# Optimization experiments

Hardware: AMD Instinct MI355X
Metric: run time of the kernel (lower is better)

The kernel has to match this reference:

```python
import jax, jax.numpy as jnp
import numpy as np
from jax.scipy.linalg import solve_triangular

SPARSITY = 5
COMMITMENT_COST = 0.25
EMBEDDING_DIM = 64
NUM_EMBEDDINGS = 512


def setup_inputs() -> dict:
    key = jax.random.key(0)
    k1, k2 = jax.random.split(key)
    z_e = jax.random.normal(k1, (64, EMBEDDING_DIM, 32, 32), dtype=jnp.float32)
    D = jax.random.normal(k2, (EMBEDDING_DIM, NUM_EMBEDDINGS), dtype=jnp.float32)
    # torch module normalizes atoms in-place (no grad through normalization)
    D = D / jnp.linalg.norm(D, axis=0)
    return {"z_e": z_e, "dictionary": D}


def _batch_omp(signals, D, sparsity):
    # signals: [C, N], D: [C, K]
    C, N = signals.shape
    dtype = signals.dtype
    G = D.T @ D                       # [K, K] Gram matrix
    init_corr = (D.T @ signals).T     # [N, K]
    corr = init_corr
    coeffs = jnp.zeros_like(init_corr)
    L = jnp.ones((N, 1, 1), dtype=dtype)
    omega = jnp.ones(init_corr.shape, dtype=bool)
    I = jnp.zeros((N, 0), dtype=jnp.int32)
    rows = jnp.arange(N)
    for k in range(1, sparsity + 1):
        # argmax atom selection (omega masks already-selected atoms)
        k_hats = jnp.argmax(jnp.abs(corr) * omega, axis=1)        # [N]
        omega = omega.at[rows, k_hats].set(False)
        if k > 1:
            # progressive Cholesky update: G_[n, j] = G[I[n, j], k_hats[n]]
            G_ = G[I, k_hats[:, None]][..., None]                  # [N, k-1, 1]
            w = solve_triangular(L, G_, lower=True)                # [N, k-1, 1]
            w_row = w.reshape(N, 1, k - 1)                         # [N, 1, k-1]
            w_br = jnp.sqrt(1.0 - jnp.sum(w_row ** 2, axis=2, keepdims=True))
            k_zeros = jnp.zeros((N, k - 1, 1), dtype=dtype)
            top = jnp.concatenate([L, k_zeros], axis=2)            # [N, k-1, k]
            bot = jnp.concatenate([w_row, w_br], axis=2)           # [N, 1, k]
            L = jnp.concatenate([top, bot], axis=1)                # [N, k, k]
        I = jnp.concatenate([I, k_hats[:, None].astype(jnp.int32)], axis=1)  # [N, k]
        b = jnp.take_along_axis(init_corr, I, axis=1)[..., None]   # [N, k, 1]
        # cholesky_solve(b, L): solve L L^T x = b
        y = solve_triangular(L, b, lower=True)
        x = solve_triangular(jnp.swapaxes(L, -1, -2), y, lower=False)  # [N, k, 1]
        xs = x[..., 0]                                             # [N, k]
        coeffs = coeffs.at[rows[:, None], I].set(xs)
        beta = jnp.einsum('nk,nkm->nm', xs, G[I])                  # [N, K]
        corr = init_corr - beta
    return coeffs.T                                                # [K, N]


def reference(z_e, dictionary):
    # z_e: [B, C, H, W] -> BHWC, then raw view as [C, B*H*W] (faithful to torch .view)
    z = jnp.transpose(z_e, (0, 2, 3, 1))
    input_shape = z.shape
    zf = z.reshape(EMBEDDING_DIM, -1)
    coeffs = _batch_omp(zf, dictionary, SPARSITY)                  # [K, N]
    z_dl = (dictionary @ coeffs).reshape(input_shape)
    e_latent_loss = jnp.mean((jax.lax.stop_gradient(z_dl) - z) ** 2)
    dl_latent_loss = jnp.mean((z_dl - jax.lax.stop_gradient(z)) ** 2)
    loss = COMMITMENT_COST * e_latent_loss + dl_latent_loss
    z_st = z + jax.lax.stop_gradient(z_dl - z)                     # straight-through
    return jnp.transpose(z_st, (0, 3, 1, 2)), loss, coeffs
```

## Files before the change

kernel.cpp:

```cpp
#include <hip/hip_runtime.h>

#define NSIG  65536
#define KAT   512
#define CDIM  64

typedef float f32x4 __attribute__((ext_vector_type(4)));

__device__ __forceinline__ f32x4 splat4(float x) { return (f32x4){x, x, x, x}; }
__device__ __forceinline__ float bcastf(float v, int l) {
  return __int_as_float(__builtin_amdgcn_readlane(__float_as_int(v), l));
}
__device__ __forceinline__ unsigned umaxu(unsigned a, unsigned b) {
  return a > b ? a : b;
}
__device__ __forceinline__ unsigned dppmax(unsigned v, const int ctrl) {
  switch (ctrl) {
    case 0xB1:  return umaxu(v, (unsigned)__builtin_amdgcn_mov_dpp((int)v, 0xB1, 0xF, 0xF, true));
    case 0x4E:  return umaxu(v, (unsigned)__builtin_amdgcn_mov_dpp((int)v, 0x4E, 0xF, 0xF, true));
    case 0x124: return umaxu(v, (unsigned)__builtin_amdgcn_mov_dpp((int)v, 0x124, 0xF, 0xF, true));
    case 0x128: return umaxu(v, (unsigned)__builtin_amdgcn_mov_dpp((int)v, 0x128, 0xF, 0xF, true));
    case 0x142: return umaxu(v, (unsigned)__builtin_amdgcn_mov_dpp((int)v, 0x142, 0xF, 0xF, true));
    default:    return umaxu(v, (unsigned)__builtin_amdgcn_mov_dpp((int)v, 0x143, 0xF, 0xF, true));
  }
}

__global__ void k_gram(const float* __restrict__ D, float* __restrict__ G,
                       float* __restrict__ DT) {
  int tid = blockIdx.x * 256 + threadIdx.x;
  int i = tid >> 9, j = tid & 511;
  float acc = 0.f;
  #pragma unroll 8
  for (int c = 0; c < CDIM; ++c) acc = fmaf(D[c * KAT + i], D[c * KAT + j], acc);
  G[tid] = acc;
  if (tid < KAT * CDIM) {
    int k = tid >> 6, c = tid & 63;
    DT[tid] = D[c * KAT + k];
  }
}

__global__ void k_tr(const float* __restrict__ ze, float* __restrict__ st) {
  __shared__ float tile[64][33];
  int cz = blockIdx.x >> 5;
  int h  = blockIdx.x & 31;
  int t  = threadIdx.x;
  #pragma unroll
  for (int q = 0; q < 8; ++q) {
    int idx = q * 256 + t;
    int b = idx >> 5, w = idx & 31;
    tile[b][w] = ze[b * 65536 + cz * 1024 + h * 32 + w];
  }
  __syncthreads();
  #pragma unroll
  for (int q = 0; q < 8; ++q) {
    int idx = q * 256 + t;
    int w = idx >> 6, b = idx & 63;
    st[(h * 2048 + w * 64 + cz) * 64 + b] = tile[b][w];
  }
}

#define DECLV(p) f32x4 p##03 = {0,0,0,0}, p##47 = {0,0,0,0}
#define FMA8V(p, sc)                                                   \
  { f32x4 s4 = splat4(sc);                                             \
    p##03 = __builtin_elementwise_fma(d03, s4, p##03);                 \
    p##47 = __builtin_elementwise_fma(d47, s4, p##47); }
#define SEL8V(e, v03, v47)                                             \
  e = v03[0];                                                          \
  e = (jj == 1) ? v03[1] : e; e = (jj == 2) ? v03[2] : e;              \
  e = (jj == 3) ? v03[3] : e; e = (jj == 4) ? v47[0] : e;              \
  e = (jj == 5) ? v47[1] : e; e = (jj == 6) ? v47[2] : e;              \
  e = (jj == 7) ? v47[3] : e

__device__ __forceinline__ float omp_one(
    f32x4& c03, f32x4& c47,
    float* __restrict__ QW,
    const float* __restrict__ G, const float* __restrict__ DT,
    float* __restrict__ coeffs,
    int n, int lane, float zv) {
  int omega = 0xFF;
  int I0 = 0, I1 = 0, I2 = 0, I3 = 0, I4 = 0;
  float L10 = 0, L20 = 0, L21 = 0;
  float L30 = 0, L31 = 0, L32 = 0;
  float L40 = 0, L41 = 0, L42 = 0, L43 = 0;
  float d1v = 1.f, d2v = 1.f, d3v = 1.f, d4v = 1.f;
  float y0v = 0, y1v = 0, y2v = 0, y3v = 0, y4v = 0;
  DECLV(Qa); DECLV(Qb); DECLV(Qc); DECLV(Qd);

  f32x4* QW4 = reinterpret_cast<f32x4*>(QW);

  #pragma unroll
  for (int it = 0; it < 5; ++it) {
    unsigned ab0 = (omega & 1)        ? (__float_as_uint(c03[0]) & 0x7FFFFFFFu) : 0u;
    unsigned ab1 = ((omega >> 1) & 1) ? (__float_as_uint(c03[1]) & 0x7FFFFFFFu) : 0u;
    unsigned ab2 = ((omega >> 2) & 1) ? (__float_as_uint(c03[2]) & 0x7FFFFFFFu) : 0u;
    unsigned ab3 = ((omega >> 3) & 1) ? (__float_as_uint(c03[3]) & 0x7FFFFFFFu) : 0u;
    unsigned ab4 = ((omega >> 4) & 1) ? (__float_as_uint(c47[0]) & 0x7FFFFFFFu) : 0u;
    unsigned ab5 = ((omega >> 5) & 1) ? (__float_as_uint(c47[1]) & 0x7FFFFFFFu) : 0u;
    unsigned ab6 = ((omega >> 6) & 1) ? (__float_as_uint(c47[2]) & 0x7FFFFFFFu) : 0u;
    unsigned ab7 = ((omega >> 7) & 1) ? (__float_as_uint(c47[3]) & 0x7FFFFFFFu) : 0u;
    unsigned la = umaxu(umaxu(umaxu(ab0, ab1), umaxu(ab2, ab3)),
                        umaxu(umaxu(ab4, ab5), umaxu(ab6, ab7)));
    unsigned rmax = la;
    rmax = dppmax(rmax, 0xB1);
    rmax = dppmax(rmax, 0x4E);
    rmax = dppmax(rmax, 0x124);
    rmax = dppmax(rmax, 0x128);
    rmax = dppmax(rmax, 0x142);
    rmax = dppmax(rmax, 0x143);
    unsigned gmu = (unsigned)__builtin_amdgcn_readlane((int)rmax, 63);
    unsigned long long ball = __ballot(la == gmu);
    const int sl = __ffsll((long long)ball) - 1;
    int jb = 7;
    jb = (ab6 == gmu) ? 6 : jb;
    jb = (ab5 == gmu) ? 5 : jb;
    jb = (ab4 == gmu) ? 4 : jb;
    jb = (ab3 == gmu) ? 3 : jb;
    jb = (ab2 == gmu) ? 2 : jb;
    jb = (ab1 == gmu) ? 1 : jb;
    jb = (ab0 == gmu) ? 0 : jb;
    const int jj = __builtin_amdgcn_readlane(jb, sl) & 7;
    const int khat = (sl << 3) | jj;
    if (lane == sl) omega &= ~(1 << jj);

    const int eoff = ((khat >> 2) & 1) * 256 + (khat >> 3) * 4 + (khat & 3);
    float w0 = 0.f, w1 = 0.f, w2 = 0.f, w3 = 0.f;
    if (it > 0) w0 = QW[eoff];
    if (it > 1) w1 = QW[512 + eoff];
    if (it > 2) w2 = QW[1024 + eoff];
    if (it > 3) { float e; SEL8V(e, Qd03, Qd47); w3 = bcastf(e, sl); }

    f32x4 na = {0, 0, 0, 0}, nbv = {0, 0, 0, 0};
    if (it < 4) {
      na  = *reinterpret_cast<const f32x4*>(G + khat * KAT + 8 * lane);
      nbv = *reinterpret_cast<const f32x4*>(G + khat * KAT + 8 * lane + 4);
    }

    float crv;
    { float e; SEL8V(e, c03, c47); crv = bcastf(e, sl); }

    float s2 = 1.f - w0 * w0 - w1 * w1 - w2 * w2 - w3 * w3;
    float dn = __builtin_amdgcn_rsqf(s2);
    float yn = crv * dn;
    if (it == 0) { I0 = khat; y0v = yn; }
    if (it == 1) { I1 = khat; y1v = yn; L10 = w0; d1v = dn; }
    if (it == 2) { I2 = khat; y2v = yn; L20 = w0; L21 = w1; d2v = dn; }
    if (it == 3) { I3 = khat; y3v = yn; L30 = w0; L31 = w1; L32 = w2; d3v = dn; }
    if (it == 4) { I4 = khat; y4v = yn; L40 = w0; L41 = w1; L42 = w2; L43 = w3; d4v = dn; }

    if (it < 4) {
      f32x4 qn03 = na, qn47 = nbv;
      if (it > 0) {
        f32x4 w4 = splat4(-w0);
        qn03 = __builtin_elementwise_fma(w4, Qa03, qn03);
        qn47 = __builtin_elementwise_fma(w4, Qa47, qn47);
      }
      if (it > 1) {
        f32x4 w4 = splat4(-w1);
        qn03 = __builtin_elementwise_fma(w4, Qb03, qn03);
        qn47 = __builtin_elementwise_fma(w4, Qb47, qn47);
      }
      if (it > 2) {
        f32x4 w4 = splat4(-w2);
        qn03 = __builtin_elementwise_fma(w4, Qc03, qn03);
        qn47 = __builtin_elementwise_fma(w4, Qc47, qn47);
      }
      f32x4 dn4 = splat4(dn);
      qn03 = qn03 * dn4;
      qn47 = qn47 * dn4;
      if (it < 3) {
        QW4[it * 128 + lane]      = qn03;
        QW4[it * 128 + 64 + lane] = qn47;
      }
      if (it == 0) { Qa03 = qn03; Qa47 = qn47; }
      if (it == 1) { Qb03 = qn03; Qb47 = qn47; }
      if (it == 2) { Qc03 = qn03; Qc47 = qn47; }
      if (it == 3) { Qd03 = qn03; Qd47 = qn47; }
      f32x4 yn4 = splat4(-yn);
      c03 = __builtin_elementwise_fma(yn4, qn03, c03);
      c47 = __builtin_elementwise_fma(yn4, qn47, c47);
    }
  }

  float x4 = y4v * d4v;
  float x3 = (y3v - L43 * x4) * d3v;
  float x2 = (y2v - L32 * x3 - L42 * x4) * d2v;
  float x1 = (y1v - L21 * x2 - L31 * x3 - L41 * x4) * d1v;
  float x0 =  y0v - L10 * x1 - L20 * x2 - L30 * x3 - L40 * x4;

  if (lane < 5) {
    int It = I0; float xt = x0;
    if (lane == 1) { It = I1; xt = x1; }
    if (lane == 2) { It = I2; xt = x2; }
    if (lane == 3) { It = I3; xt = x3; }
    if (lane == 4) { It = I4; xt = x4; }
    coeffs[(long)It * NSIG + n] = xt;
  }
  float rec = x0 * DT[I0 * 64 + lane];
  rec = fmaf(x1, DT[I1 * 64 + lane], rec);
  rec = fmaf(x2, DT[I2 * 64 + lane], rec);
  rec = fmaf(x3, DT[I3 * 64 + lane], rec);
  rec = fmaf(x4, DT[I4 * 64 + lane], rec);
  return rec - zv;
}

__global__ __launch_bounds__(64) void k_omp(
    const float* __restrict__ D, const float* __restrict__ G,
    const float* __restrict__ DT, const float* __restrict__ ST,
    float* __restrict__ out0, float* __restrict__ lossp,
    float* __restrict__ coeffs) {
  __shared__ float QL[3][512];
  const int lane = threadIdx.x;
  const int wid  = blockIdx.x;
  const int cc = wid >> 7;
  const int w3 = wid & 127;
  const int nbase = cc + 512 * w3;
  const float* Dp = D + 8 * lane;
  float* QW = &QL[0][0];
  float lossacc = 0.f;

  const int n0 = nbase;             const int n1 = nbase + 64;
  const int n2 = nbase + 128;       const int n3 = nbase + 192;
  const int n4 = nbase + 256;       const int n5 = nbase + 320;
  const int n6 = nbase + 384;       const int n7 = nbase + 448;
  float svA = ST[n0 * 64 + lane];
  float svB = ST[n1 * 64 + lane];
  float svC = ST[n2 * 64 + lane];
  float svD = ST[n3 * 64 + lane];
  float svE = ST[n4 * 64 + lane];
  float svF = ST[n5 * 64 + lane];
  float svG = ST[n6 * 64 + lane];
  float svH = ST[n7 * 64 + lane];

  DECLV(cA); DECLV(cB); DECLV(cC); DECLV(cD);
  DECLV(cE); DECLV(cF); DECLV(cG); DECLV(cH);

  #pragma unroll 2
  for (int r = 0; r < 64; ++r) {
    const f32x4 d03 = *reinterpret_cast<const f32x4*>(Dp + r * KAT);
    const f32x4 d47 = *reinterpret_cast<const f32x4*>(Dp + r * KAT + 4);
    const float sA = bcastf(svA, r);
    const float sB = bcastf(svB, r);
    const float sC = bcastf(svC, r);
    const float sD = bcastf(svD, r);
    const float sE = bcastf(svE, r);
    const float sF = bcastf(svF, r);
    const float sG = bcastf(svG, r);
    const float sH = bcastf(svH, r);
    FMA8V(cA, sA) FMA8V(cB, sB) FMA8V(cC, sC) FMA8V(cD, sD)
    FMA8V(cE, sE) FMA8V(cF, sF) FMA8V(cG, sG) FMA8V(cH, sH)
  }

  float dA = omp_one(cA03, cA47, QW, G, DT, coeffs, n0, lane, svA);
  lossacc = fmaf(dA, dA, lossacc);
  float dB = omp_one(cB03, cB47, QW, G, DT, coeffs, n1, lane, svB);
  lossacc = fmaf(dB, dB, lossacc);
  float dC = omp_one(cC03, cC47, QW, G, DT, coeffs, n2, lane, svC);
  lossacc = fmaf(dC, dC, lossacc);
  float dD = omp_one(cD03, cD47, QW, G, DT, coeffs, n3, lane, svD);
  lossacc = fmaf(dD, dD, lossacc);
  float dE = omp_one(cE03, cE47, QW, G, DT, coeffs, n4, lane, svE);
  lossacc = fmaf(dE, dE, lossacc);
  float dF = omp_one(cF03, cF47, QW, G, DT, coeffs, n5, lane, svF);
  lossacc = fmaf(dF, dF, lossacc);
  float dG = omp_one(cG03, cG47, QW, G, DT, coeffs, n6, lane, svG);
  lossacc = fmaf(dG, dG, lossacc);
  float dH = omp_one(cH03, cH47, QW, G, DT, coeffs, n7, lane, svH);
  lossacc = fmaf(dH, dH, lossacc);

  const int obase = lane * 65536 + cc * 1024 + (w3 >> 2) * 32 + (w3 & 3) * 8;
  *reinterpret_cast<float4*>(out0 + obase) =
      make_float4(svA + dA, svB + dB, svC + dC, svD + dD);
  *reinterpret_cast<float4*>(out0 + obase + 4) =
      make_float4(svE + dE, svF + dF, svG + dG, svH + dH);

  #pragma unroll
  for (int off = 32; off > 0; off >>= 1) lossacc += __shfl_xor(lossacc, off);
  if (lane == 0) atomicAdd(lossp, lossacc * (1.25f / 4194304.f));
}

extern "C" void kernel_launch(void* const* d_in, const int* in_sizes, int n_in,
                              void* d_out, int out_size, void* d_ws, size_t ws_size,
                              hipStream_t stream) {
  const float* ze = (const float*)d_in[0];
  const float* D  = (const float*)d_in[1];
  float* out0 = (float*)d_out;
  float* lossp = out0 + 4194304;
  float* coeffs = out0 + 4194305;

  float* wsf = (float*)d_ws;
  float* G  = wsf;
  float* DT = wsf + 262144;
  float* ST = wsf + 294912;

  (void)hipMemsetAsync((char*)d_out + 16777216ull, 0, 134217732ull, stream);

  hipLaunchKernelGGL(k_gram, dim3(1024), dim3(256), 0, stream, D, G, DT);
  hipLaunchKernelGGL(k_tr,   dim3(2048), dim3(256), 0, stream, ze, ST);
  hipLaunchKernelGGL(k_omp,  dim3(8192), dim3(64), 0, stream,
                     D, G, DT, ST, out0, lossp, coeffs);
}
```

Measured before the change: 173.8 us.

## Process two signals per wavefront, one per 32-lane half, in OMP kernel

Splits each 64-lane wavefront into two halves that each run OMP for a separate signal, with every lane holding 16 correlations instead of 8. The argmax reduction stops at 32 lanes, and Q vectors from earlier iterations now live in shared memory instead of registers. The aim is to halve the serial OMP iteration chains per wave and cut the reduction steps. In exchange each lane does twice the per-element work, shared-memory traffic grows, and register pressure may rise.

```diff
diff --git a/kernel.cpp b/kernel.cpp
--- a/kernel.cpp
+++ b/kernel.cpp
@@ -9,6 +9,9 @@
 __device__ __forceinline__ f32x4 splat4(float x) { return (f32x4){x, x, x, x}; }
 __device__ __forceinline__ float bcastf(float v, int l) {
   return __int_as_float(__builtin_amdgcn_readlane(__float_as_int(v), l));
+}
+__device__ __forceinline__ int bcasti(int v, int l) {
+  return __builtin_amdgcn_readlane(v, l);
 }
 __device__ __forceinline__ unsigned umaxu(unsigned a, unsigned b) {
   return a > b ? a : b;
@@ -19,8 +22,7 @@
     case 0x4E:  return umaxu(v, (unsigned)__builtin_amdgcn_mov_dpp((int)v, 0x4E, 0xF, 0xF, true));
     case 0x124: return umaxu(v, (unsigned)__builtin_amdgcn_mov_dpp((int)v, 0x124, 0xF, 0xF, true));
     case 0x128: return umaxu(v, (unsigned)__builtin_amdgcn_mov_dpp((int)v, 0x128, 0xF, 0xF, true));
-    case 0x142: return umaxu(v, (unsigned)__builtin_amdgcn_mov_dpp((int)v, 0x142, 0xF, 0xF, true));
-    default:    return umaxu(v, (unsigned)__builtin_amdgcn_mov_dpp((int)v, 0x143, 0xF, 0xF, true));
+    default:    return umaxu(v, (unsigned)__builtin_amdgcn_mov_dpp((int)v, 0x142, 0xF, 0xF, true));
   }
 }
 
@@ -58,125 +60,172 @@
   }
 }
 
-#define DECLV(p) f32x4 p##03 = {0,0,0,0}, p##47 = {0,0,0,0}
-#define FMA8V(p, sc)                                                   \
-  { f32x4 s4 = splat4(sc);                                             \
-    p##03 = __builtin_elementwise_fma(d03, s4, p##03);                 \
-    p##47 = __builtin_elementwise_fma(d47, s4, p##47); }
-#define SEL8V(e, v03, v47)                                             \
-  e = v03[0];                                                          \
-  e = (jj == 1) ? v03[1] : e; e = (jj == 2) ? v03[2] : e;              \
-  e = (jj == 3) ? v03[3] : e; e = (jj == 4) ? v47[0] : e;              \
-  e = (jj == 5) ? v47[1] : e; e = (jj == 6) ? v47[2] : e;              \
-  e = (jj == 7) ? v47[3] : e
-
-__device__ __forceinline__ float omp_one(
-    f32x4& c03, f32x4& c47,
+#define SEL16(e, v0, v1, v2, v3, idx)                                   \
+  e = v0[0];                                                            \
+  e = ((idx) == 1) ? v0[1] : e;  e = ((idx) == 2) ? v0[2] : e;          \
+  e = ((idx) == 3) ? v0[3] : e;  e = ((idx) == 4) ? v1[0] : e;          \
+  e = ((idx) == 5) ? v1[1] : e;  e = ((idx) == 6) ? v1[2] : e;          \
+  e = ((idx) == 7) ? v1[3] : e;  e = ((idx) == 8) ? v2[0] : e;          \
+  e = ((idx) == 9) ? v2[1] : e;  e = ((idx) == 10) ? v2[2] : e;         \
+  e = ((idx) == 11) ? v2[3] : e; e = ((idx) == 12) ? v3[0] : e;         \
+  e = ((idx) == 13) ? v3[1] : e; e = ((idx) == 14) ? v3[2] : e;         \
+  e = ((idx) == 15) ? v3[3] : e;
+
+__device__ __forceinline__ void omp_pair(
+    f32x4& c0, f32x4& c1, f32x4& c2, f32x4& c3,
     float* __restrict__ QW,
     const float* __restrict__ G, const float* __restrict__ DT,
     float* __restrict__ coeffs,
-    int n, int lane, float zv) {
-  int omega = 0xFF;
-  int I0 = 0, I1 = 0, I2 = 0, I3 = 0, I4 = 0;
-  float L10 = 0, L20 = 0, L21 = 0;
-  float L30 = 0, L31 = 0, L32 = 0;
-  float L40 = 0, L41 = 0, L42 = 0, L43 = 0;
-  float d1v = 1.f, d2v = 1.f, d3v = 1.f, d4v = 1.f;
-  float y0v = 0, y1v = 0, y2v = 0, y3v = 0, y4v = 0;
-  DECLV(Qa); DECLV(Qb); DECLV(Qc); DECLV(Qd);
+    int nP, int nQ, int lane, float svP, float svQ,
+    float& dP_out, float& dQ_out) {
+  const int hl = lane & 31;
+  const bool loHalf = lane < 32;
+  const int sb4 = loHalf ? 0 : 384;
+  unsigned omega = 0xFFFFu;
+  int IA0=0, IA1=0, IA2=0, IA3=0, IA4=0;
+  int IB0=0, IB1=0, IB2=0, IB3=0, IB4=0;
+  float L10=0, L20=0, L21=0, L30=0, L31=0, L32=0;
+  float L40=0, L41=0, L42=0, L43=0;
+  float d1v=1.f, d2v=1.f, d3v=1.f, d4v=1.f;
+  float y0v=0, y1v=0, y2v=0, y3v=0, y4v=0;
+  f32x4 Qd0={0,0,0,0}, Qd1={0,0,0,0}, Qd2={0,0,0,0}, Qd3={0,0,0,0};
 
   f32x4* QW4 = reinterpret_cast<f32x4*>(QW);
 
   #pragma unroll
   for (int it = 0; it < 5; ++it) {
-    unsigned ab0 = (omega & 1)        ? (__float_as_uint(c03[0]) & 0x7FFFFFFFu) : 0u;
-    unsigned ab1 = ((omega >> 1) & 1) ? (__float_as_uint(c03[1]) & 0x7FFFFFFFu) : 0u;
-    unsigned ab2 = ((omega >> 2) & 1) ? (__float_as_uint(c03[2]) & 0x7FFFFFFFu) : 0u;
-    unsigned ab3 = ((omega >> 3) & 1) ? (__float_as_uint(c03[3]) & 0x7FFFFFFFu) : 0u;
-    unsigned ab4 = ((omega >> 4) & 1) ? (__float_as_uint(c47[0]) & 0x7FFFFFFFu) : 0u;
-    unsigned ab5 = ((omega >> 5) & 1) ? (__float_as_uint(c47[1]) & 0x7FFFFFFFu) : 0u;
-    unsigned ab6 = ((omega >> 6) & 1) ? (__float_as_uint(c47[2]) & 0x7FFFFFFFu) : 0u;
-    unsigned ab7 = ((omega >> 7) & 1) ? (__float_as_uint(c47[3]) & 0x7FFFFFFFu) : 0u;
-    unsigned la = umaxu(umaxu(umaxu(ab0, ab1), umaxu(ab2, ab3)),
-                        umaxu(umaxu(ab4, ab5), umaxu(ab6, ab7)));
+    unsigned ab0  = (omega & 1u)          ? (__float_as_uint(c0[0]) & 0x7FFFFFFFu) : 0u;
+    unsigned ab1  = ((omega >> 1) & 1u)   ? (__float_as_uint(c0[1]) & 0x7FFFFFFFu) : 0u;
+    unsigned ab2  = ((omega >> 2) & 1u)   ? (__float_as_uint(c0[2]) & 0x7FFFFFFFu) : 0u;
+    unsigned ab3  = ((omega >> 3) & 1u)   ? (__float_as_uint(c0[3]) & 0x7FFFFFFFu) : 0u;
+    unsigned ab4  = ((omega >> 4) & 1u)   ? (__float_as_uint(c1[0]) & 0x7FFFFFFFu) : 0u;
+    unsigned ab5  = ((omega >> 5) & 1u)   ? (__float_as_uint(c1[1]) & 0x7FFFFFFFu) : 0u;
+    unsigned ab6  = ((omega >> 6) & 1u)   ? (__float_as_uint(c1[2]) & 0x7FFFFFFFu) : 0u;
+    unsigned ab7  = ((omega >> 7) & 1u)   ? (__float_as_uint(c1[3]) & 0x7FFFFFFFu) : 0u;
+    unsigned ab8  = ((omega >> 8) & 1u)   ? (__float_as_uint(c2[0]) & 0x7FFFFFFFu) : 0u;
+    unsigned ab9  = ((omega >> 9) & 1u)   ? (__float_as_uint(c2[1]) & 0x7FFFFFFFu) : 0u;
+    unsigned ab10 = ((omega >> 10) & 1u)  ? (__float_as_uint(c2[2]) & 0x7FFFFFFFu) : 0u;
+    unsigned ab11 = ((omega >> 11) & 1u)  ? (__float_as_uint(c2[3]) & 0x7FFFFFFFu) : 0u;
+    unsigned ab12 = ((omega >> 12) & 1u)  ? (__float_as_uint(c3[0]) & 0x7FFFFFFFu) : 0u;
+    unsigned ab13 = ((omega >> 13) & 1u)  ? (__float_as_uint(c3[1]) & 0x7FFFFFFFu) : 0u;
+    unsigned ab14 = ((omega >> 14) & 1u)  ? (__float_as_uint(c3[2]) & 0x7FFFFFFFu) : 0u;
+    unsigned ab15 = ((omega >> 15) & 1u)  ? (__float_as_uint(c3[3]) & 0x7FFFFFFFu) : 0u;
+    unsigned la = umaxu(
+        umaxu(umaxu(umaxu(ab0, ab1), umaxu(ab2, ab3)),
+              umaxu(umaxu(ab4, ab5), umaxu(ab6, ab7))),
+        umaxu(umaxu(umaxu(ab8, ab9), umaxu(ab10, ab11)),
+              umaxu(umaxu(ab12, ab13), umaxu(ab14, ab15))));
     unsigned rmax = la;
     rmax = dppmax(rmax, 0xB1);
     rmax = dppmax(rmax, 0x4E);
     rmax = dppmax(rmax, 0x124);
     rmax = dppmax(rmax, 0x128);
     rmax = dppmax(rmax, 0x142);
-    rmax = dppmax(rmax, 0x143);
-    unsigned gmu = (unsigned)__builtin_amdgcn_readlane((int)rmax, 63);
+    unsigned gA = (unsigned)bcasti((int)rmax, 31);
+    unsigned gB = (unsigned)bcasti((int)rmax, 63);
+    unsigned gmu = loHalf ? gA : gB;
     unsigned long long ball = __ballot(la == gmu);
-    const int sl = __ffsll((long long)ball) - 1;
-    int jb = 7;
-    jb = (ab6 == gmu) ? 6 : jb;
-    jb = (ab5 == gmu) ? 5 : jb;
-    jb = (ab4 == gmu) ? 4 : jb;
-    jb = (ab3 == gmu) ? 3 : jb;
-    jb = (ab2 == gmu) ? 2 : jb;
-    jb = (ab1 == gmu) ? 1 : jb;
-    jb = (ab0 == gmu) ? 0 : jb;
-    const int jj = __builtin_amdgcn_readlane(jb, sl) & 7;
-    const int khat = (sl << 3) | jj;
-    if (lane == sl) omega &= ~(1 << jj);
-
-    const int eoff = ((khat >> 2) & 1) * 256 + (khat >> 3) * 4 + (khat & 3);
+    const int slA = __ffsll((long long)(ball & 0xFFFFFFFFull)) - 1;
+    const int slB = 32 + __ffsll((long long)(ball >> 32)) - 1;
+    int jb = 15;
+    jb = (ab14 == gmu) ? 14 : jb;
+    jb = (ab13 == gmu) ? 13 : jb;
+    jb = (ab12 == gmu) ? 12 : jb;
+    jb = (ab11 == gmu) ? 11 : jb;
+    jb = (ab10 == gmu) ? 10 : jb;
+    jb = (ab9  == gmu) ? 9  : jb;
+    jb = (ab8  == gmu) ? 8  : jb;
+    jb = (ab7  == gmu) ? 7  : jb;
+    jb = (ab6  == gmu) ? 6  : jb;
+    jb = (ab5  == gmu) ? 5  : jb;
+    jb = (ab4  == gmu) ? 4  : jb;
+    jb = (ab3  == gmu) ? 3  : jb;
+    jb = (ab2  == gmu) ? 2  : jb;
+    jb = (ab1  == gmu) ? 1  : jb;
+    jb = (ab0  == gmu) ? 0  : jb;
+    const int jjA = bcasti(jb, slA) & 15;
+    const int jjB = bcasti(jb, slB) & 15;
+    const int khatA = ((slA & 31) << 4) | jjA;
+    const int khatB = ((slB & 31) << 4) | jjB;
+    if (lane == slA || lane == slB) omega &= ~(1u << (jb & 15));
+
+    const int eoffA = ((khatA & 15) >> 2) * 128 + (khatA >> 4) * 4 + (khatA & 3);
+    const int eoffB = ((khatB & 15) >> 2) * 128 + (khatB >> 4) * 4 + (khatB & 3);
+    const int hbase = loHalf ? eoffA : (1536 + eoffB);
     float w0 = 0.f, w1 = 0.f, w2 = 0.f, w3 = 0.f;
-    if (it > 0) w0 = QW[eoff];
-    if (it > 1) w1 = QW[512 + eoff];
-    if (it > 2) w2 = QW[1024 + eoff];
-    if (it > 3) { float e; SEL8V(e, Qd03, Qd47); w3 = bcastf(e, sl); }
-
-    f32x4 na = {0, 0, 0, 0}, nbv = {0, 0, 0, 0};
+    if (it > 0) w0 = QW[hbase];
+    if (it > 1) w1 = QW[hbase + 512];
+    if (it > 2) w2 = QW[hbase + 1024];
+    if (it > 3) {
+      float e; SEL16(e, Qd0, Qd1, Qd2, Qd3, jb)
+      float eA = bcastf(e, slA), eB = bcastf(e, slB);
+      w3 = loHalf ? eA : eB;
+    }
+
+    const int khat_l = loHalf ? khatA : khatB;
+    const float* Gp = G + khat_l * KAT + hl * 16;
+    f32x4 na = {0,0,0,0}, nb = {0,0,0,0}, nc = {0,0,0,0}, nd = {0,0,0,0};
     if (it < 4) {
-      na  = *reinterpret_cast<const f32x4*>(G + khat * KAT + 8 * lane);
-      nbv = *reinterpret_cast<const f32x4*>(G + khat * KAT + 8 * lane + 4);
+      na = *reinterpret_cast<const f32x4*>(Gp);
+      nb = *reinterpret_cast<const f32x4*>(Gp + 4);
+      nc = *reinterpret_cast<const f32x4*>(Gp + 8);
+      nd = *reinterpret_cast<const f32x4*>(Gp + 12);
     }
 
     float crv;
-    { float e; SEL8V(e, c03, c47); crv = bcastf(e, sl); }
-
-    float s2 = 1.f - w0 * w0 - w1 * w1 - w2 * w2 - w3 * w3;
-    float dn = __builtin_amdgcn_rsqf(s2);
+    {
+      float e; SEL16(e, c0, c1, c2, c3, jb)
+      float eA = bcastf(e, slA), eB = bcastf(e, slB);
+      crv = loHalf ? eA : eB;
+    }
+
+    float s2v = 1.f - w0 * w0 - w1 * w1 - w2 * w2 - w3 * w3;
+    float dn = __builtin_amdgcn_rsqf(s2v);
     float yn = crv * dn;
-    if (it == 0) { I0 = khat; y0v = yn; }
-    if (it == 1) { I1 = khat; y1v = yn; L10 = w0; d1v = dn; }
-    if (it == 2) { I2 = khat; y2v = yn; L20 = w0; L21 = w1; d2v = dn; }
-    if (it == 3) { I3 = khat; y3v = yn; L30 = w0; L31 = w1; L32 = w2; d3v = dn; }
-    if (it == 4) { I4 = khat; y4v = yn; L40 = w0; L41 = w1; L42 = w2; L43 = w3; d4v = dn; }
+    if (it == 0) { IA0 = khatA; IB0 = khatB; y0v = yn; }
+    if (it == 1) { IA1 = khatA; IB1 = khatB; y1v = yn; L10 = w0; d1v = dn; }
+    if (it == 2) { IA2 = khatA; IB2 = khatB; y2v = yn; L20 = w0; L21 = w1; d2v = dn; }
+    if (it == 3) { IA3 = khatA; IB3 = khatB; y3v = yn; L30 = w0; L31 = w1; L32 = w2; d3v = dn; }
+    if (it == 4) { IA4 = khatA; IB4 = khatB; y4v = yn; L40 = w0; L41 = w1; L42 = w2; L43 = w3; d4v = dn; }
 
     if (it < 4) {
-      f32x4 qn03 = na, qn47 = nbv;
+      f32x4 qn0 = na, qn1 = nb, qn2 = nc, qn3 = nd;
       if (it > 0) {
         f32x4 w4 = splat4(-w0);
-        qn03 = __builtin_elementwise_fma(w4, Qa03, qn03);
-        qn47 = __builtin_elementwise_fma(w4, Qa47, qn47);
+        qn0 = __builtin_elementwise_fma(w4, QW4[sb4 + 0 * 32 + hl], qn0);
+        qn1 = __builtin_elementwise_fma(w4, QW4[sb4 + 1 * 32 + hl], qn1);
+        qn2 = __builtin_elementwise_fma(w4, QW4[sb4 + 2 * 32 + hl], qn2);
+        qn3 = __builtin_elementwise_fma(w4, QW4[sb4 + 3 * 32 + hl], qn3);
       }
       if (it > 1) {
         f32x4 w4 = splat4(-w1);
-        qn03 = __builtin_elementwise_fma(w4, Qb03, qn03);
-        qn47 = __builtin_elementwise_fma(w4, Qb47, qn47);
+        qn0 = __builtin_elementwise_fma(w4, QW4[sb4 + 128 + 0 * 32 + hl], qn0);
+        qn1 = __builtin_elementwise_fma(w4, QW4[sb4 + 128 + 1 * 32 + hl], qn1);
+        qn2 = __builtin_elementwise_fma(w4, QW4[sb4 + 128 + 2 * 32 + hl], qn2);
+        qn3 = __builtin_elementwise_fma(w4, QW4[sb4 + 128 + 3 * 32 + hl], qn3);
       }
       if (it > 2) {
         f32x4 w4 = splat4(-w2);
-        qn03 = __builtin_elementwise_fma(w4, Qc03, qn03);
-        qn47 = __builtin_elementwise_fma(w4, Qc47, qn47);
+        qn0 = __builtin_elementwise_fma(w4, QW4[sb4 + 256 + 0 * 32 + hl], qn0);
+        qn1 = __builtin_elementwise_fma(w4, QW4[sb4 + 256 + 1 * 32 + hl], qn1);
+        qn2 = __builtin_elementwise_fma(w4, QW4[sb4 + 256 + 2 * 32 + hl], qn2);
+        qn3 = __builtin_elementwise_fma(w4, QW4[sb4 + 256 + 3 * 32 + hl], qn3);
       }
       f32x4 dn4 = splat4(dn);
-      qn03 = qn03 * dn4;
-      qn47 = qn47 * dn4;
+      qn0 = qn0 * dn4; qn1 = qn1 * dn4; qn2 = qn2 * dn4; qn3 = qn3 * dn4;
       if (it < 3) {
-        QW4[it * 128 + lane]      = qn03;
-        QW4[it * 128 + 64 + lane] = qn47;
+        QW4[sb4 + it * 128 + 0 * 32 + hl] = qn0;
+        QW4[sb4 + it * 128 + 1 * 32 + hl] = qn1;
+        QW4[sb4 + it * 128 + 2 * 32 + hl] = qn2;
+        QW4[sb4 + it * 128 + 3 * 32 + hl] = qn3;
+      } else {
+        Qd0 = qn0; Qd1 = qn1; Qd2 = qn2; Qd3 = qn3;
       }
-      if (it == 0) { Qa03 = qn03; Qa47 = qn47; }
-      if (it == 1) { Qb03 = qn03; Qb47 = qn47; }
-      if (it == 2) { Qc03 = qn03; Qc47 = qn47; }
-      if (it == 3) { Qd03 = qn03; Qd47 = qn47; }
       f32x4 yn4 = splat4(-yn);
-      c03 = __builtin_elementwise_fma(yn4, qn03, c03);
-      c47 = __builtin_elementwise_fma(yn4, qn47, c47);
+      c0 = __builtin_elementwise_fma(yn4, qn0, c0);
+      c1 = __builtin_elementwise_fma(yn4, qn1, c1);
+      c2 = __builtin_elementwise_fma(yn4, qn2, c2);
+      c3 = __builtin_elementwise_fma(yn4, qn3, c3);
     }
   }
 
@@ -186,35 +235,64 @@
   float x1 = (y1v - L21 * x2 - L31 * x3 - L41 * x4) * d1v;
   float x0 =  y0v - L10 * x1 - L20 * x2 - L30 * x3 - L40 * x4;
 
-  if (lane < 5) {
-    int It = I0; float xt = x0;
-    if (lane == 1) { It = I1; xt = x1; }
-    if (lane == 2) { It = I2; xt = x2; }
-    if (lane == 3) { It = I3; xt = x3; }
-    if (lane == 4) { It = I4; xt = x4; }
-    coeffs[(long)It * NSIG + n] = xt;
-  }
-  float rec = x0 * DT[I0 * 64 + lane];
-  rec = fmaf(x1, DT[I1 * 64 + lane], rec);
-  rec = fmaf(x2, DT[I2 * 64 + lane], rec);
-  rec = fmaf(x3, DT[I3 * 64 + lane], rec);
-  rec = fmaf(x4, DT[I4 * 64 + lane], rec);
-  return rec - zv;
-}
+  {
+    const int ll = lane & 31;
+    if (ll < 5) {
+      int ItA = IA0;
+      ItA = (ll == 1) ? IA1 : ItA; ItA = (ll == 2) ? IA2 : ItA;
+      ItA = (ll == 3) ? IA3 : ItA; ItA = (ll == 4) ? IA4 : ItA;
+      int ItB = IB0;
+      ItB = (ll == 1) ? IB1 : ItB; ItB = (ll == 2) ? IB2 : ItB;
+      ItB = (ll == 3) ? IB3 : ItB; ItB = (ll == 4) ? IB4 : ItB;
+      const int It = loHalf ? ItA : ItB;
+      float xt = x0;
+      xt = (ll == 1) ? x1 : xt; xt = (ll == 2) ? x2 : xt;
+      xt = (ll == 3) ? x3 : xt; xt = (ll == 4) ? x4 : xt;
+      const int nn = loHalf ? nP : nQ;
+      coeffs[(long)It * NSIG + nn] = xt;
+    }
+  }
+
+  const float xA0 = bcastf(x0, 0),  xA1 = bcastf(x1, 0),  xA2 = bcastf(x2, 0);
+  const float xA3 = bcastf(x3, 0),  xA4 = bcastf(x4, 0);
+  const float xB0 = bcastf(x0, 32), xB1 = bcastf(x1, 32), xB2 = bcastf(x2, 32);
+  const float xB3 = bcastf(x3, 32), xB4 = bcastf(x4, 32);
+  float recP = xA0 * DT[IA0 * 64 + lane];
+  recP = fmaf(xA1, DT[IA1 * 64 + lane], recP);
+  recP = fmaf(xA2, DT[IA2 * 64 + lane], recP);
+  recP = fmaf(xA3, DT[IA3 * 64 + lane], recP);
+  recP = fmaf(xA4, DT[IA4 * 64 + lane], recP);
+  float recQ = xB0 * DT[IB0 * 64 + lane];
+  recQ = fmaf(xB1, DT[IB1 * 64 + lane], recQ);
+  recQ = fmaf(xB2, DT[IB2 * 64 + lane], recQ);
+  recQ = fmaf(xB3, DT[IB3 * 64 + lane], recQ);
+  recQ = fmaf(xB4, DT[IB4 * 64 + lane], recQ);
+  dP_out = recP - svP;
+  dQ_out = recQ - svQ;
+}
+
+#define DECLV4(p) f32x4 p##0 = {0,0,0,0}, p##1 = {0,0,0,0}, p##2 = {0,0,0,0}, p##3 = {0,0,0,0}
+#define FMA16V(p, cv)                                          \
+  { f32x4 s4 = splat4(cv);                                     \
+    p##0 = __builtin_elementwise_fma(da, s4, p##0);            \
+    p##1 = __builtin_elementwise_fma(db, s4, p##1);            \
+    p##2 = __builtin_elementwise_fma(dc, s4, p##2);            \
+    p##3 = __builtin_elementwise_fma(dd, s4, p##3); }
 
 __global__ __launch_bounds__(64) void k_omp(
     const float* __restrict__ D, const float* __restrict__ G,
     const float* __restrict__ DT, const float* __restrict__ ST,
     float* __restrict__ out0, float* __restrict__ lossp,
     float* __restrict__ coeffs) {
-  __shared__ float QL[3][512];
+  __shared__ float QL[2][3][512];
   const int lane = threadIdx.x;
+  const int hl = lane & 31;
+  const bool loHalf = lane < 32;
   const int wid  = blockIdx.x;
   const int cc = wid >> 7;
   const int w3 = wid & 127;
   const int nbase = cc + 512 * w3;
-  const float* Dp = D + 8 * lane;
-  float* QW = &QL[0][0];
+  float* QW = &QL[0][0][0];
   float lossacc = 0.f;
 
   const int n0 = nbase;             const int n1 = nbase + 64;
@@ -230,41 +308,31 @@
   float svG = ST[n6 * 64 + lane];
   float svH = ST[n7 * 64 + lane];
 
-  DECLV(cA); DECLV(cB); DECLV(cC); DECLV(cD);
-  DECLV(cE); DECLV(cF); DECLV(cG); DECLV(cH);
+  DECLV4(pAB); DECLV4(pCD); DECLV4(pEF); DECLV4(pGH);
+  const float* Dq = D + hl * 16;
 
   #pragma unroll 2
   for (int r = 0; r < 64; ++r) {
-    const f32x4 d03 = *reinterpret_cast<const f32x4*>(Dp + r * KAT);
-    const f32x4 d47 = *reinterpret_cast<const f32x4*>(Dp + r * KAT + 4);
-    const float sA = bcastf(svA, r);
-    const float sB = bcastf(svB, r);
-    const float sC = bcastf(svC, r);
-    const float sD = bcastf(svD, r);
-    const float sE = bcastf(svE, r);
-    const float sF = bcastf(svF, r);
-    const float sG = bcastf(svG, r);
-    const float sH = bcastf(svH, r);
-    FMA8V(cA, sA) FMA8V(cB, sB) FMA8V(cC, sC) FMA8V(cD, sD)
-    FMA8V(cE, sE) FMA8V(cF, sF) FMA8V(cG, sG) FMA8V(cH, sH)
-  }
-
-  float dA = omp_one(cA03, cA47, QW, G, DT, coeffs, n0, lane, svA);
-  lossacc = fmaf(dA, dA, lossacc);
-  float dB = omp_one(cB03, cB47, QW, G, DT, coeffs, n1, lane, svB);
-  lossacc = fmaf(dB, dB, lossacc);
-  float dC = omp_one(cC03, cC47, QW, G, DT, coeffs, n2, lane, svC);
-  lossacc = fmaf(dC, dC, lossacc);
-  float dD = omp_one(cD03, cD47, QW, G, DT, coeffs, n3, lane, svD);
-  lossacc = fmaf(dD, dD, lossacc);
-  float dE = omp_one(cE03, cE47, QW, G, DT, coeffs, n4, lane, svE);
-  lossacc = fmaf(dE, dE, lossacc);
-  float dF = omp_one(cF03, cF47, QW, G, DT, coeffs, n5, lane, svF);
-  lossacc = fmaf(dF, dF, lossacc);
-  float dG = omp_one(cG03, cG47, QW, G, DT, coeffs, n6, lane, svG);
-  lossacc = fmaf(dG, dG, lossacc);
-  float dH = omp_one(cH03, cH47, QW, G, DT, coeffs, n7, lane, svH);
-  lossacc = fmaf(dH, dH, lossacc);
+    const f32x4 da = *reinterpret_cast<const f32x4*>(Dq + r * KAT);
+    const f32x4 db = *reinterpret_cast<const f32x4*>(Dq + r * KAT + 4);
+    const f32x4 dc = *reinterpret_cast<const f32x4*>(Dq + r * KAT + 8);
+    const f32x4 dd = *reinterpret_cast<const f32x4*>(Dq + r * KAT + 12);
+    const float v01 = loHalf ? bcastf(svA, r) : bcastf(svB, r);
+    const float v23 = loHalf ? bcastf(svC, r) : bcastf(svD, r);
+    const float v45 = loHalf ? bcastf(svE, r) : bcastf(svF, r);
+    const float v67 = loHalf ? bcastf(svG, r) : bcastf(svH, r);
+    FMA16V(pAB, v01) FMA16V(pCD, v23) FMA16V(pEF, v45) FMA16V(pGH, v67)
+  }
+
+  float dA, dB, dC, dD, dE, dF, dG, dH;
+  omp_pair(pAB0, pAB1, pAB2, pAB3, QW, G, DT, coeffs, n0, n1, lane, svA, svB, dA, dB);
+  lossacc = fmaf(dA, dA, fmaf(dB, dB, lossacc));
+  omp_pair(pCD0, pCD1, pCD2, pCD3, QW, G, DT, coeffs, n2, n3, lane, svC, svD, dC, dD);
+  lossacc = fmaf(dC, dC, fmaf(dD, dD, lossacc));
+  omp_pair(pEF0, pEF1, pEF2, pEF3, QW, G, DT, coeffs, n4, n5, lane, svE, svF, dE, dF);
+  lossacc = fmaf(dE, dE, fmaf(dF, dF, lossacc));
+  omp_pair(pGH0, pGH1, pGH2, pGH3, QW, G, DT, coeffs, n6, n7, lane, svG, svH, dG, dH);
+  lossacc = fmaf(dG, dG, fmaf(dH, dH, lossacc));
 
   const int obase = lane * 65536 + cc * 1024 + (w3 >> 2) * 32 + (w3 & 3) * 8;
   *reinterpret_cast<float4*>(out0 + obase) =
```

After: 250.2 us. +44.0%, slower.
